# Optimization experiments

Hardware: AMD Instinct MI355X
Metric: run time of the kernel (lower is better)

Reference implementation:

```python
import jax, jax.numpy as jnp
import numpy as np
import math

NUM_HEADS = 32
NUM_KV_HEADS = 8
HEAD_DIM = 64
ROPE_THETA = 150000.0


def rotate_half(x):
    half = x.shape[-1] // 2
    return jnp.concatenate([-x[..., half:], x[..., :half]], axis=-1)


def setup_inputs() -> dict:
    key = jax.random.key(0)
    k1, k2, k3, k4, k5 = jax.random.split(key, 5)
    B, S, H = 2, 2048, 2048
    qkv_size = (NUM_HEADS + 2 * NUM_KV_HEADS) * HEAD_DIM  # 3072
    scale = 1.0 / math.sqrt(H)
    return {
        "hidden_states": jax.random.normal(k1, (B, S, H), jnp.float32),
        "position_ids": jnp.arange(S, dtype=jnp.int64 if jax.config.jax_enable_x64 else jnp.int32)[None, :],
        "qkv_w": jax.random.normal(k2, (qkv_size, H), jnp.float32) * scale,
        "qkv_b": jax.random.normal(k3, (qkv_size,), jnp.float32) * 0.01,
        "o_w": jax.random.normal(k4, (H, NUM_HEADS * HEAD_DIM), jnp.float32) * scale,
        "o_b": jax.random.normal(k5, (H,), jnp.float32) * 0.01,
    }


def reference(hidden_states, position_ids, qkv_w, qkv_b, o_w, o_b):
    B, S, _ = hidden_states.shape
    g = NUM_HEADS // NUM_KV_HEADS  # query heads per kv head
    d = HEAD_DIM

    qkv = hidden_states @ qkv_w.T + qkv_b  # [B,S,(H+2KV)*d]
    qkv = qkv.reshape(B, S, NUM_KV_HEADS, g + 2, d)
    q = qkv[:, :, :, :g, :].reshape(B, S, NUM_HEADS, d).transpose(0, 2, 1, 3)   # [B,Hq,S,d]
    k = qkv[:, :, :, g, :].transpose(0, 2, 1, 3)                                 # [B,Hkv,S,d]
    v = qkv[:, :, :, g + 1, :].transpose(0, 2, 1, 3)                             # [B,Hkv,S,d]

    # HF-style RoPE: cos/sin [S, d]
    inv_freq = 1.0 / (ROPE_THETA ** (jnp.arange(0, d, 2, dtype=jnp.float32) / d))
    freqs = jnp.outer(position_ids.reshape(-1).astype(jnp.float32), inv_freq)    # [S, d/2]
    emb = jnp.concatenate([freqs, freqs], axis=-1)                               # [S, d]
    cos = jnp.cos(emb)[None, None]                                               # [1,1,S,d]
    sin = jnp.sin(emb)[None, None]
    q = q * cos + rotate_half(q) * sin
    k = k * cos + rotate_half(k) * sin

    # GQA: repeat_interleave kv heads to match query heads
    k = jnp.repeat(k, g, axis=1)  # [B,Hq,S,d]
    v = jnp.repeat(v, g, axis=1)

    scores = jnp.einsum("bhqd,bhkd->bhqk", q, k) / math.sqrt(d)  # [B,Hq,S,S]
    attn = jax.nn.softmax(scores, axis=-1)
    out = jnp.einsum("bhqk,bhkd->bhqd", attn, v)
    out = out.transpose(0, 2, 1, 3).reshape(B, S, NUM_HEADS * d)
    return out @ o_w.T + o_b
```

## Files before the change

### kernel.cpp

```cpp
#include <hip/hip_runtime.h>
#include <math.h>

#define NHQ 32
#define NKV 8
#define HD 64
#define QKV_DIM 3072
#define MODEL_DIM 2048
#define QSCALE 0.1803368801111204f

typedef __attribute__((ext_vector_type(4))) float     f32x4;
typedef __attribute__((ext_vector_type(8))) _Float16  half8;
typedef __attribute__((ext_vector_type(4))) _Float16  half4v;
typedef __attribute__((ext_vector_type(2))) __fp16    fp16x2;
typedef __attribute__((ext_vector_type(4))) unsigned  uint32x4;

#define ASYNC_COPY16(g, l)                                                        \
    __builtin_amdgcn_global_load_lds(                                             \
        (const __attribute__((address_space(1))) void*)(g),                       \
        (__attribute__((address_space(3))) void*)(l), 16, 0, 0)

__device__ __forceinline__ float fast_exp2(float x)
{
#if __has_builtin(__builtin_amdgcn_exp2f)
    return __builtin_amdgcn_exp2f(x);
#else
    float r;
    asm volatile("v_exp_f32 %0, %1\ns_nop 0" : "=v"(r) : "v"(x));
    return r;
#endif
}

__global__ __launch_bounds__(256)
void f32_to_f16_kernel(const float* __restrict__ src, _Float16* __restrict__ dst, int n4)
{
    int i = blockIdx.x * 256 + threadIdx.x;
    if (i < n4) {
        float4 v = ((const float4*)src)[i];
        half4v h = { (_Float16)v.x, (_Float16)v.y, (_Float16)v.z, (_Float16)v.w };
        ((half4v*)dst)[i] = h;
    }
}

__global__ __launch_bounds__(256)
void sincos_table_kernel(const int* __restrict__ pos, float* __restrict__ tab, int S)
{
    int i = blockIdx.x * 256 + threadIdx.x;
    if (i < S * 32) {
        int s = i >> 5, fi = i & 31;
        float p = (float)pos[s];
        float inv_freq = powf(150000.0f, -(float)fi * (1.0f / 32.0f));
        float ang = p * inv_freq;
        tab[s * 64 + fi]      = cosf(ang);
        tab[s * 64 + 32 + fi] = sinf(ang);
    }
}

template<int MODE>
__global__ __launch_bounds__(256, 3)
void gemm_f16_mfma(const _Float16* __restrict__ A, const _Float16* __restrict__ W,
                   const float* __restrict__ bias, void* __restrict__ Cout,
                   const float* __restrict__ tab, int M, int N, int K, int S)
{
    __shared__ _Float16 As[3][128 * 32];
    __shared__ _Float16 Bs[3][128 * 32];

    const int t    = threadIdx.x;
    const int w    = t >> 6;
    const int lane = t & 63;
    const int quad = lane >> 4, l15 = lane & 15;
    const size_t m0 = (size_t)blockIdx.y * 128;
    const size_t n0 = (size_t)blockIdx.x * 128;
    const int wm = (w >> 1) * 64, wn = (w & 1) * 64;

    const int sr   = t >> 2;
    const int klog = ((t & 3) ^ ((sr >> 1) & 3)) * 8;
    const _Float16* ag0 = A + (m0 + sr) * K + klog;
    const _Float16* ag1 = A + (m0 + 64 + sr) * K + klog;
    const _Float16* bg0 = W + (n0 + sr) * K + klog;
    const _Float16* bg1 = W + (n0 + 64 + sr) * K + klog;

    const int xk8 = (quad ^ ((l15 >> 1) & 3)) * 8;

    f32x4 acc[4][4];
#pragma unroll
    for (int i = 0; i < 4; i++)
#pragma unroll
        for (int j = 0; j < 4; j++) acc[i][j] = (f32x4){0.f, 0.f, 0.f, 0.f};

    const int nt = K >> 5;

#define STAGE_TILE(bi, kt_)                                         \
    do {                                                            \
        const int _k0 = (kt_) * 32;                                 \
        ASYNC_COPY16(ag0 + _k0, &As[bi][w * 512]);                  \
        ASYNC_COPY16(ag1 + _k0, &As[bi][2048 + w * 512]);           \
        ASYNC_COPY16(bg0 + _k0, &Bs[bi][w * 512]);                  \
        ASYNC_COPY16(bg1 + _k0, &Bs[bi][2048 + w * 512]);           \
    } while (0)

    STAGE_TILE(0, 0);
    STAGE_TILE(1, 1);
    asm volatile("s_waitcnt vmcnt(4)" ::: "memory");
    __builtin_amdgcn_s_barrier();
    __builtin_amdgcn_sched_barrier(0);

    int bc = 0;
    for (int kt = 0; kt < nt; ++kt) {
        const _Float16* Ab = &As[bc][0];
        const _Float16* Bb = &Bs[bc][0];

        half8 af[4], bf[4];
#pragma unroll
        for (int i = 0; i < 4; i++) {
            af[i] = *(const half8*)(Ab + (wm + i * 16 + l15) * 32 + xk8);
            bf[i] = *(const half8*)(Bb + (wn + i * 16 + l15) * 32 + xk8);
        }

        if (kt + 2 < nt) {
            int bs = bc + 2; if (bs >= 3) bs -= 3;
            STAGE_TILE(bs, kt + 2);
        }

        __builtin_amdgcn_s_setprio(1);
#pragma unroll
        for (int i = 0; i < 4; i++)
#pragma unroll
            for (int j = 0; j < 4; j++)
                acc[i][j] = __builtin_amdgcn_mfma_f32_16x16x32_f16(af[i], bf[j], acc[i][j], 0, 0, 0);
        __builtin_amdgcn_s_setprio(0);

        if (kt + 1 < nt) {
            if (kt + 2 < nt) asm volatile("s_waitcnt vmcnt(4)" ::: "memory");
            else             asm volatile("s_waitcnt vmcnt(0)" ::: "memory");
            __builtin_amdgcn_s_barrier();
            __builtin_amdgcn_sched_barrier(0);
        }
        bc = bc + 1; if (bc == 3) bc = 0;
    }
#undef STAGE_TILE

    float bv[4];
#pragma unroll
    for (int j = 0; j < 4; j++) bv[j] = bias[n0 + wn + j * 16 + l15];

    const int ct = (int)(((n0 + wn) >> 6) % 6);

#pragma unroll
    for (int i = 0; i < 4; i++)
#pragma unroll
        for (int r = 0; r < 4; r++) {
            const size_t row = m0 + wm + i * 16 + quad * 4 + r;
            float v[4];
#pragma unroll
            for (int j = 0; j < 4; j++) v[j] = acc[i][j][r] + bv[j];

            if (MODE == 2 && ct != 5) {
                const float* tc = tab + (size_t)(row % S) * 64;
                const float ca = tc[l15],      sa = tc[32 + l15];
                const float cb = tc[16 + l15], sb = tc[48 + l15];
                const float qs = (ct < 4) ? QSCALE : 1.0f;
                const float n0v = v[0] * ca - v[2] * sa;
                const float n1v = v[1] * cb - v[3] * sb;
                const float n2v = v[2] * ca + v[0] * sa;
                const float n3v = v[3] * cb + v[1] * sb;
                v[0] = n0v * qs; v[1] = n1v * qs; v[2] = n2v * qs; v[3] = n3v * qs;
            }

            const size_t col = n0 + wn + l15;
#pragma unroll
            for (int j = 0; j < 4; j++) {
                if (MODE != 0) ((_Float16*)Cout)[row * N + col + j * 16] = (_Float16)v[j];
                else           ((float*)Cout)[row * N + col + j * 16] = v[j];
            }
        }
}

__global__ __launch_bounds__(256)
void transpose_v_kernel(const _Float16* __restrict__ qkv, _Float16* __restrict__ vtg, int BS)
{
    __shared__ _Float16 tile[64 * 72];
    const int t = threadIdx.x;
    const int tb = blockIdx.x * 64;
    const int g = blockIdx.y;
    const int voff = (g * 6 + 5) * 64;

    const int tok = t >> 2, dsub = (t & 3) * 16;
    const _Float16* src = qkv + (size_t)(tb + tok) * QKV_DIM + voff + dsub;
    *(half8*)&tile[tok * 72 + dsub]     = *(const half8*)(src);
    *(half8*)&tile[tok * 72 + dsub + 8] = *(const half8*)(src + 8);
    __syncthreads();

    const int d = t >> 2, tsub = (t & 3) * 16;
    half8 a, c;
#pragma unroll
    for (int i = 0; i < 8; i++) a[i] = tile[(tsub + i) * 72 + d];
#pragma unroll
    for (int i = 0; i < 8; i++) c[i] = tile[(tsub + 8 + i) * 72 + d];
    _Float16* dst = vtg + ((size_t)g * 64 + d) * BS + tb + tsub;
    *(half8*)dst       = a;
    *(half8*)(dst + 8) = c;
}

__global__ __launch_bounds__(256)
void attn_mfma(const _Float16* __restrict__ qkv, const _Float16* __restrict__ vtg,
               _Float16* __restrict__ out, int B, int S)
{
    __shared__ _Float16 Ks[64 * 72];
    __shared__ _Float16 VsT[64 * 72];

    const int t = threadIdx.x, w = t >> 6, lane = t & 63;
    const int quad = lane >> 4, l15 = lane & 15;
    const int b = blockIdx.z, g = blockIdx.y;
    const int q0 = blockIdx.x * 32;
    const int qoff = (g * 6 + w) * 64;
    const int koff = (g * 6 + 4) * 64;

    half8 qf[2][2];
#pragma unroll
    for (int s = 0; s < 2; s++) {
        const _Float16* qp = qkv + (size_t)(b * S + q0 + s * 16 + l15) * QKV_DIM + qoff;
        qf[s][0] = *(const half8*)(qp + quad * 8);
        qf[s][1] = *(const half8*)(qp + 32 + quad * 8);
    }

    half8 lv;
    {
        const _Float16 one = (l15 == 0) ? (_Float16)1.0f : (_Float16)0.0f;
#pragma unroll
        for (int j = 0; j < 8; j++) lv[j] = one;
    }

    f32x4 O[2][4], L[2];
#pragma unroll
    for (int s = 0; s < 2; s++) {
        L[s] = (f32x4){0.f, 0.f, 0.f, 0.f};
#pragma unroll
        for (int dt = 0; dt < 4; dt++) O[s][dt] = (f32x4){0.f, 0.f, 0.f, 0.f};
    }

    const int kst_tok = t >> 2;
    const int kst_d   = (t & 3) * 16;
    const int vst_d   = t >> 3;
    const int vst_sub = (t & 7) * 8;

    const _Float16* kbase  = qkv + (size_t)(b * S + kst_tok) * QKV_DIM + koff + kst_d;
    const _Float16* vbase0 = vtg + ((size_t)g * 64 + vst_d) * (size_t)(B * S) + b * S + vst_sub;
    const _Float16* vbase1 = vtg + ((size_t)g * 64 + 32 + vst_d) * (size_t)(B * S) + b * S + vst_sub;

    half8 kr0 = *(const half8*)(kbase);
    half8 kr1 = *(const half8*)(kbase + 8);
    half8 vr0 = *(const half8*)(vbase0);
    half8 vr1 = *(const half8*)(vbase1);

    for (int kt = 0; kt < S; kt += 64) {
        *(half8*)&Ks[kst_tok * 72 + kst_d]         = kr0;
        *(half8*)&Ks[kst_tok * 72 + kst_d + 8]     = kr1;
        *(half8*)&VsT[vst_d * 72 + vst_sub]        = vr0;
        *(half8*)&VsT[(32 + vst_d) * 72 + vst_sub] = vr1;
        __syncthreads();

        if (kt + 64 < S) {
            kr0 = *(const half8*)(kbase + (size_t)(kt + 64) * QKV_DIM);
            kr1 = *(const half8*)(kbase + (size_t)(kt + 64) * QKV_DIM + 8);
            vr0 = *(const half8*)(vbase0 + kt + 64);
            vr1 = *(const half8*)(vbase1 + kt + 64);
        }

        half8 kf[4][2];
#pragma unroll
        for (int mt = 0; mt < 4; mt++) {
            kf[mt][0] = *(const half8*)&Ks[(mt * 16 + l15) * 72 + quad * 8];
            kf[mt][1] = *(const half8*)&Ks[(mt * 16 + l15) * 72 + 32 + quad * 8];
        }

        half8 pf[2][2];
#pragma unroll
        for (int s = 0; s < 2; s++) {
            f32x4 sacc[4];
#pragma unroll
            for (int mt = 0; mt < 4; mt++) {
                f32x4 z = (f32x4){0.f, 0.f, 0.f, 0.f};
                z = __builtin_amdgcn_mfma_f32_16x16x32_f16(kf[mt][0], qf[s][0], z, 0, 0, 0);
                z = __builtin_amdgcn_mfma_f32_16x16x32_f16(kf[mt][1], qf[s][1], z, 0, 0, 0);
                sacc[mt] = z;
            }

            unsigned u[4][2];
#pragma unroll
            for (int mt = 0; mt < 4; mt++) {
                fp16x2 pa = __builtin_amdgcn_cvt_pkrtz(fast_exp2(sacc[mt][0]),
                                                       fast_exp2(sacc[mt][1]));
                fp16x2 pb = __builtin_amdgcn_cvt_pkrtz(fast_exp2(sacc[mt][2]),
                                                       fast_exp2(sacc[mt][3]));
                u[mt][0] = __builtin_bit_cast(unsigned, pa);
                u[mt][1] = __builtin_bit_cast(unsigned, pb);
            }

#pragma unroll
            for (int h = 0; h < 2; h++) {
                uint32x4 pw;
#pragma unroll
                for (int c = 0; c < 2; c++) {
                    unsigned x = u[h * 2][c], y = u[h * 2 + 1][c];
                    asm("v_permlane32_swap_b32 %0, %1" : "+v"(x), "+v"(y));
                    asm("v_permlane16_swap_b32 %0, %1" : "+v"(x), "+v"(y));
                    pw[c]     = x;
                    pw[2 + c] = y;
                }
                pf[s][h] = __builtin_bit_cast(half8, pw);
            }
        }

#pragma unroll
        for (int dt = 0; dt < 4; dt++) {
            half8 vv0 = *(const half8*)&VsT[(dt * 16 + l15) * 72 + quad * 8];
            half8 vv1 = *(const half8*)&VsT[(dt * 16 + l15) * 72 + 32 + quad * 8];
#pragma unroll
            for (int s = 0; s < 2; s++) {
                O[s][dt] = __builtin_amdgcn_mfma_f32_16x16x32_f16(pf[s][0], vv0, O[s][dt], 0, 0, 0);
                O[s][dt] = __builtin_amdgcn_mfma_f32_16x16x32_f16(pf[s][1], vv1, O[s][dt], 0, 0, 0);
            }
        }
#pragma unroll
        for (int s = 0; s < 2; s++) {
            L[s] = __builtin_amdgcn_mfma_f32_16x16x32_f16(pf[s][0], lv, L[s], 0, 0, 0);
            L[s] = __builtin_amdgcn_mfma_f32_16x16x32_f16(pf[s][1], lv, L[s], 0, 0, 0);
        }
        __syncthreads();
    }

    const int hq = g * 4 + w;
#pragma unroll
    for (int s = 0; s < 2; s++)
#pragma unroll
        for (int r = 0; r < 4; r++) {
            const float lr = __shfl(L[s][r], lane & 48, 64);
            const float ir = 1.0f / lr;
            const size_t row = (size_t)(b * S + q0 + s * 16 + quad * 4 + r);
#pragma unroll
            for (int dt = 0; dt < 4; dt++)
                out[row * (NHQ * HD) + hq * 64 + dt * 16 + l15] = (_Float16)(O[s][dt][r] * ir);
        }
}

extern "C" void kernel_launch(void* const* d_in, const int* in_sizes, int n_in,
                              void* d_out, int out_size, void* d_ws, size_t ws_size,
                              hipStream_t stream)
{
    const float* hidden = (const float*)d_in[0];
    const int*   pos    = (const int*)d_in[1];
    const float* qkv_w  = (const float*)d_in[2];
    const float* qkv_b  = (const float*)d_in[3];
    const float* o_w    = (const float*)d_in[4];
    const float* o_b    = (const float*)d_in[5];
    float* out = (float*)d_out;

    const int S  = in_sizes[1];
    const int BS = in_sizes[0] / MODEL_DIM;
    const int B  = BS / S;

    _Float16* hA   = (_Float16*)d_ws;
    _Float16* hW1  = hA   + (size_t)BS * MODEL_DIM;
    _Float16* hW2  = hW1  + (size_t)QKV_DIM * MODEL_DIM;
    _Float16* qkvh = hW2  + (size_t)MODEL_DIM * MODEL_DIM;
    _Float16* atth = qkvh + (size_t)BS * QKV_DIM;
    float*    tab  = (float*)(atth + (size_t)BS * MODEL_DIM);
    _Float16* vtg  = (_Float16*)(tab + (size_t)S * 64);

    f32_to_f16_kernel<<<(BS * MODEL_DIM / 4 + 255) / 256, 256, 0, stream>>>(hidden, hA, BS * MODEL_DIM / 4);
    f32_to_f16_kernel<<<(QKV_DIM * MODEL_DIM / 4 + 255) / 256, 256, 0, stream>>>(qkv_w, hW1, QKV_DIM * MODEL_DIM / 4);
    f32_to_f16_kernel<<<(MODEL_DIM * MODEL_DIM / 4 + 255) / 256, 256, 0, stream>>>(o_w, hW2, MODEL_DIM * MODEL_DIM / 4);
    sincos_table_kernel<<<(S * 32 + 255) / 256, 256, 0, stream>>>(pos, tab, S);

    gemm_f16_mfma<2><<<dim3(QKV_DIM / 128, BS / 128), 256, 0, stream>>>(
        hA, hW1, qkv_b, qkvh, tab, BS, QKV_DIM, MODEL_DIM, S);

    transpose_v_kernel<<<dim3(BS / 64, NKV), 256, 0, stream>>>(qkvh, vtg, BS);

    attn_mfma<<<dim3(S / 32, NKV, B), 256, 0, stream>>>(qkvh, vtg, atth, B, S);

    gemm_f16_mfma<0><<<dim3(MODEL_DIM / 128, BS / 128), 256, 0, stream>>>(
        atth, hW2, o_b, out, nullptr, BS, MODEL_DIM, MODEL_DIM, S);
}
```

Before: 314.9 us.

## Double-buffer attention K/V tiles, add MFMA priority hints, swizzle GEMM tile order

The attention kernel now keeps two LDS buffers for K and V^T. The next tile is written into the spare buffer while the current one is used for compute, which removes one __syncthreads per iteration and prefetches two tiles ahead. s_setprio is raised around the MFMA sections so the waves doing matrix work get scheduled first. The GEMM remaps block IDs using an XCD-aware interleave followed by grouped-M tile ordering, aiming for better L2 reuse across chiplets. Doubling LDS raises the attention kernel's shared-memory footprint, which could reduce occupancy.

```diff
diff --git a/kernel.cpp b/kernel.cpp
--- a/kernel.cpp
+++ b/kernel.cpp
@@ -68,8 +68,21 @@
     const int w    = t >> 6;
     const int lane = t & 63;
     const int quad = lane >> 4, l15 = lane & 15;
-    const size_t m0 = (size_t)blockIdx.y * 128;
-    const size_t n0 = (size_t)blockIdx.x * 128;
+
+    const int nnt = gridDim.x, nmt = gridDim.y;
+    int id = blockIdx.y * nnt + blockIdx.x;
+    const int nwg = nnt * nmt;
+    id = (id & 7) * (nwg >> 3) + (id >> 3);
+    const int GM  = 8;
+    const int npg = GM * nnt;
+    const int grp = id / npg;
+    const int fm  = grp * GM;
+    const int gsz = (nmt - fm < GM) ? (nmt - fm) : GM;
+    const int mtl = fm + (id % gsz);
+    const int ntl = (id % npg) / gsz;
+    const size_t m0 = (size_t)mtl * 128;
+    const size_t n0 = (size_t)ntl * 128;
+
     const int wm = (w >> 1) * 64, wn = (w & 1) * 64;
 
     const int sr   = t >> 2;
@@ -87,7 +100,7 @@
 #pragma unroll
         for (int j = 0; j < 4; j++) acc[i][j] = (f32x4){0.f, 0.f, 0.f, 0.f};
 
-    const int nt = K >> 5;
+    const int nkt = K >> 5;
 
 #define STAGE_TILE(bi, kt_)                                         \
     do {                                                            \
@@ -105,7 +118,7 @@
     __builtin_amdgcn_sched_barrier(0);
 
     int bc = 0;
-    for (int kt = 0; kt < nt; ++kt) {
+    for (int kt = 0; kt < nkt; ++kt) {
         const _Float16* Ab = &As[bc][0];
         const _Float16* Bb = &Bs[bc][0];
 
@@ -116,7 +129,7 @@
             bf[i] = *(const half8*)(Bb + (wn + i * 16 + l15) * 32 + xk8);
         }
 
-        if (kt + 2 < nt) {
+        if (kt + 2 < nkt) {
             int bs = bc + 2; if (bs >= 3) bs -= 3;
             STAGE_TILE(bs, kt + 2);
         }
@@ -129,8 +142,8 @@
                 acc[i][j] = __builtin_amdgcn_mfma_f32_16x16x32_f16(af[i], bf[j], acc[i][j], 0, 0, 0);
         __builtin_amdgcn_s_setprio(0);
 
-        if (kt + 1 < nt) {
-            if (kt + 2 < nt) asm volatile("s_waitcnt vmcnt(4)" ::: "memory");
+        if (kt + 1 < nkt) {
+            if (kt + 2 < nkt) asm volatile("s_waitcnt vmcnt(4)" ::: "memory");
             else             asm volatile("s_waitcnt vmcnt(0)" ::: "memory");
             __builtin_amdgcn_s_barrier();
             __builtin_amdgcn_sched_barrier(0);
@@ -205,8 +218,8 @@
 void attn_mfma(const _Float16* __restrict__ qkv, const _Float16* __restrict__ vtg,
                _Float16* __restrict__ out, int B, int S)
 {
-    __shared__ _Float16 Ks[64 * 72];
-    __shared__ _Float16 VsT[64 * 72];
+    __shared__ _Float16 Ks[2][64 * 72];
+    __shared__ _Float16 VsT[2][64 * 72];
 
     const int t = threadIdx.x, w = t >> 6, lane = t & 63;
     const int quad = lane >> 4, l15 = lane & 15;
@@ -251,32 +264,46 @@
     half8 kr1 = *(const half8*)(kbase + 8);
     half8 vr0 = *(const half8*)(vbase0);
     half8 vr1 = *(const half8*)(vbase1);
+    *(half8*)&Ks[0][kst_tok * 72 + kst_d]         = kr0;
+    *(half8*)&Ks[0][kst_tok * 72 + kst_d + 8]     = kr1;
+    *(half8*)&VsT[0][vst_d * 72 + vst_sub]        = vr0;
+    *(half8*)&VsT[0][(32 + vst_d) * 72 + vst_sub] = vr1;
+    __syncthreads();
+    if (64 < S) {
+        kr0 = *(const half8*)(kbase + (size_t)64 * QKV_DIM);
+        kr1 = *(const half8*)(kbase + (size_t)64 * QKV_DIM + 8);
+        vr0 = *(const half8*)(vbase0 + 64);
+        vr1 = *(const half8*)(vbase1 + 64);
+    }
 
     for (int kt = 0; kt < S; kt += 64) {
-        *(half8*)&Ks[kst_tok * 72 + kst_d]         = kr0;
-        *(half8*)&Ks[kst_tok * 72 + kst_d + 8]     = kr1;
-        *(half8*)&VsT[vst_d * 72 + vst_sub]        = vr0;
-        *(half8*)&VsT[(32 + vst_d) * 72 + vst_sub] = vr1;
-        __syncthreads();
+        const int c = (kt >> 6) & 1;
 
         if (kt + 64 < S) {
-            kr0 = *(const half8*)(kbase + (size_t)(kt + 64) * QKV_DIM);
-            kr1 = *(const half8*)(kbase + (size_t)(kt + 64) * QKV_DIM + 8);
-            vr0 = *(const half8*)(vbase0 + kt + 64);
-            vr1 = *(const half8*)(vbase1 + kt + 64);
+            *(half8*)&Ks[c ^ 1][kst_tok * 72 + kst_d]         = kr0;
+            *(half8*)&Ks[c ^ 1][kst_tok * 72 + kst_d + 8]     = kr1;
+            *(half8*)&VsT[c ^ 1][vst_d * 72 + vst_sub]        = vr0;
+            *(half8*)&VsT[c ^ 1][(32 + vst_d) * 72 + vst_sub] = vr1;
+        }
+        if (kt + 128 < S) {
+            kr0 = *(const half8*)(kbase + (size_t)(kt + 128) * QKV_DIM);
+            kr1 = *(const half8*)(kbase + (size_t)(kt + 128) * QKV_DIM + 8);
+            vr0 = *(const half8*)(vbase0 + kt + 128);
+            vr1 = *(const half8*)(vbase1 + kt + 128);
         }
 
         half8 kf[4][2];
 #pragma unroll
         for (int mt = 0; mt < 4; mt++) {
-            kf[mt][0] = *(const half8*)&Ks[(mt * 16 + l15) * 72 + quad * 8];
-            kf[mt][1] = *(const half8*)&Ks[(mt * 16 + l15) * 72 + 32 + quad * 8];
+            kf[mt][0] = *(const half8*)&Ks[c][(mt * 16 + l15) * 72 + quad * 8];
+            kf[mt][1] = *(const half8*)&Ks[c][(mt * 16 + l15) * 72 + 32 + quad * 8];
         }
 
         half8 pf[2][2];
 #pragma unroll
         for (int s = 0; s < 2; s++) {
             f32x4 sacc[4];
+            __builtin_amdgcn_s_setprio(1);
 #pragma unroll
             for (int mt = 0; mt < 4; mt++) {
                 f32x4 z = (f32x4){0.f, 0.f, 0.f, 0.f};
@@ -284,6 +311,7 @@
                 z = __builtin_amdgcn_mfma_f32_16x16x32_f16(kf[mt][1], qf[s][1], z, 0, 0, 0);
                 sacc[mt] = z;
             }
+            __builtin_amdgcn_s_setprio(0);
 
             unsigned u[4][2];
 #pragma unroll
@@ -300,21 +328,22 @@
             for (int h = 0; h < 2; h++) {
                 uint32x4 pw;
 #pragma unroll
-                for (int c = 0; c < 2; c++) {
-                    unsigned x = u[h * 2][c], y = u[h * 2 + 1][c];
+                for (int cc = 0; cc < 2; cc++) {
+                    unsigned x = u[h * 2][cc], y = u[h * 2 + 1][cc];
                     asm("v_permlane32_swap_b32 %0, %1" : "+v"(x), "+v"(y));
                     asm("v_permlane16_swap_b32 %0, %1" : "+v"(x), "+v"(y));
-                    pw[c]     = x;
-                    pw[2 + c] = y;
+                    pw[cc]     = x;
+                    pw[2 + cc] = y;
                 }
                 pf[s][h] = __builtin_bit_cast(half8, pw);
             }
         }
 
+        __builtin_amdgcn_s_setprio(1);
 #pragma unroll
         for (int dt = 0; dt < 4; dt++) {
-            half8 vv0 = *(const half8*)&VsT[(dt * 16 + l15) * 72 + quad * 8];
-            half8 vv1 = *(const half8*)&VsT[(dt * 16 + l15) * 72 + 32 + quad * 8];
+            half8 vv0 = *(const half8*)&VsT[c][(dt * 16 + l15) * 72 + quad * 8];
+            half8 vv1 = *(const half8*)&VsT[c][(dt * 16 + l15) * 72 + 32 + quad * 8];
 #pragma unroll
             for (int s = 0; s < 2; s++) {
                 O[s][dt] = __builtin_amdgcn_mfma_f32_16x16x32_f16(pf[s][0], vv0, O[s][dt], 0, 0, 0);
@@ -326,6 +355,8 @@
             L[s] = __builtin_amdgcn_mfma_f32_16x16x32_f16(pf[s][0], lv, L[s], 0, 0, 0);
             L[s] = __builtin_amdgcn_mfma_f32_16x16x32_f16(pf[s][1], lv, L[s], 0, 0, 0);
         }
+        __builtin_amdgcn_s_setprio(0);
+
         __syncthreads();
     }
 
```

Measured after the change: 323.6 us. 1.03x slower.

## Deepen GEMM LDS pipeline to four stages with register double-buffered fragments

Applied to the files above, without the earlier changes.

The GEMM moves from a 3-stage to a 4-stage LDS ring, prefetching three tiles ahead, and double-buffers the MFMA fragments in registers so the next tile's LDS reads overlap the current MFMAs. The loop is unrolled by two to alternate fragment buffers. The three fp32-to-fp16 conversion launches are merged into one kernel to save launch overhead. In exchange the kernel uses more LDS and registers, and the occupancy hint of 3 blocks per CU is dropped.

```diff
diff --git a/kernel.cpp b/kernel.cpp
--- a/kernel.cpp
+++ b/kernel.cpp
@@ -31,14 +31,26 @@
 }
 
 __global__ __launch_bounds__(256)
-void f32_to_f16_kernel(const float* __restrict__ src, _Float16* __restrict__ dst, int n4)
-{
-    int i = blockIdx.x * 256 + threadIdx.x;
-    if (i < n4) {
-        float4 v = ((const float4*)src)[i];
-        half4v h = { (_Float16)v.x, (_Float16)v.y, (_Float16)v.z, (_Float16)v.w };
-        ((half4v*)dst)[i] = h;
-    }
+void convert3_kernel(const float* __restrict__ s0, _Float16* __restrict__ d0, int n0,
+                     const float* __restrict__ s1, _Float16* __restrict__ d1, int n1,
+                     const float* __restrict__ s2, _Float16* __restrict__ d2, int n2)
+{
+    int j = blockIdx.x * 256 + threadIdx.x;
+    const float* s;
+    _Float16* d;
+    if (j < n0) { s = s0; d = d0; }
+    else {
+        j -= n0;
+        if (j < n1) { s = s1; d = d1; }
+        else {
+            j -= n1;
+            if (j >= n2) return;
+            s = s2; d = d2;
+        }
+    }
+    float4 v = ((const float4*)s)[j];
+    half4v h = { (_Float16)v.x, (_Float16)v.y, (_Float16)v.z, (_Float16)v.w };
+    ((half4v*)d)[j] = h;
 }
 
 __global__ __launch_bounds__(256)
@@ -56,13 +68,13 @@
 }
 
 template<int MODE>
-__global__ __launch_bounds__(256, 3)
+__global__ __launch_bounds__(256)
 void gemm_f16_mfma(const _Float16* __restrict__ A, const _Float16* __restrict__ W,
                    const float* __restrict__ bias, void* __restrict__ Cout,
                    const float* __restrict__ tab, int M, int N, int K, int S)
 {
-    __shared__ _Float16 As[3][128 * 32];
-    __shared__ _Float16 Bs[3][128 * 32];
+    __shared__ _Float16 As[4][128 * 32];
+    __shared__ _Float16 Bs[4][128 * 32];
 
     const int t    = threadIdx.x;
     const int w    = t >> 6;
@@ -87,7 +99,7 @@
 #pragma unroll
         for (int j = 0; j < 4; j++) acc[i][j] = (f32x4){0.f, 0.f, 0.f, 0.f};
 
-    const int nt = K >> 5;
+    const int nkt = K >> 5;
 
 #define STAGE_TILE(bi, kt_)                                         \
     do {                                                            \
@@ -98,45 +110,51 @@
         ASYNC_COPY16(bg1 + _k0, &Bs[bi][2048 + w * 512]);           \
     } while (0)
 
+#define LOAD_FRAGS(F, bi)                                                     \
+    do {                                                                      \
+        const _Float16* _Ab = &As[bi][0];                                     \
+        const _Float16* _Bb = &Bs[bi][0];                                     \
+        _Pragma("unroll")                                                     \
+        for (int i = 0; i < 4; i++) {                                         \
+            F[i]     = *(const half8*)(_Ab + (wm + i * 16 + l15) * 32 + xk8); \
+            F[4 + i] = *(const half8*)(_Bb + (wn + i * 16 + l15) * 32 + xk8); \
+        }                                                                     \
+    } while (0)
+
+#define KBODY(FC, FN, k)                                                      \
+    do {                                                                      \
+        if ((k) + 3 < nkt) STAGE_TILE(((k) + 3) & 3, (k) + 3);                \
+        if ((k) + 1 < nkt) LOAD_FRAGS(FN, ((k) + 1) & 3);                     \
+        __builtin_amdgcn_s_setprio(1);                                        \
+        _Pragma("unroll")                                                     \
+        for (int i = 0; i < 4; i++)                                           \
+            _Pragma("unroll")                                                 \
+            for (int j = 0; j < 4; j++)                                       \
+                acc[i][j] = __builtin_amdgcn_mfma_f32_16x16x32_f16(           \
+                    FC[i], FC[4 + j], acc[i][j], 0, 0, 0);                    \
+        __builtin_amdgcn_s_setprio(0);                                        \
+        if ((k) + 1 < nkt) {                                                  \
+            if ((k) + 3 < nkt) asm volatile("s_waitcnt vmcnt(4)" ::: "memory"); \
+            else               asm volatile("s_waitcnt vmcnt(0)" ::: "memory"); \
+            __builtin_amdgcn_s_barrier();                                     \
+            __builtin_amdgcn_sched_barrier(0);                                \
+        }                                                                     \
+    } while (0)
+
     STAGE_TILE(0, 0);
     STAGE_TILE(1, 1);
-    asm volatile("s_waitcnt vmcnt(4)" ::: "memory");
-    __builtin_amdgcn_s_barrier();
-    __builtin_amdgcn_sched_barrier(0);
-
-    int bc = 0;
-    for (int kt = 0; kt < nt; ++kt) {
-        const _Float16* Ab = &As[bc][0];
-        const _Float16* Bb = &Bs[bc][0];
-
-        half8 af[4], bf[4];
-#pragma unroll
-        for (int i = 0; i < 4; i++) {
-            af[i] = *(const half8*)(Ab + (wm + i * 16 + l15) * 32 + xk8);
-            bf[i] = *(const half8*)(Bb + (wn + i * 16 + l15) * 32 + xk8);
-        }
-
-        if (kt + 2 < nt) {
-            int bs = bc + 2; if (bs >= 3) bs -= 3;
-            STAGE_TILE(bs, kt + 2);
-        }
-
-        __builtin_amdgcn_s_setprio(1);
-#pragma unroll
-        for (int i = 0; i < 4; i++)
-#pragma unroll
-            for (int j = 0; j < 4; j++)
-                acc[i][j] = __builtin_amdgcn_mfma_f32_16x16x32_f16(af[i], bf[j], acc[i][j], 0, 0, 0);
-        __builtin_amdgcn_s_setprio(0);
-
-        if (kt + 1 < nt) {
-            if (kt + 2 < nt) asm volatile("s_waitcnt vmcnt(4)" ::: "memory");
-            else             asm volatile("s_waitcnt vmcnt(0)" ::: "memory");
-            __builtin_amdgcn_s_barrier();
-            __builtin_amdgcn_sched_barrier(0);
-        }
-        bc = bc + 1; if (bc == 3) bc = 0;
-    }
+    STAGE_TILE(2, 2);
+    __syncthreads();
+
+    half8 fA[8], fB[8];
+    LOAD_FRAGS(fA, 0);
+
+    for (int k = 0; k < nkt; k += 2) {
+        KBODY(fA, fB, k);
+        KBODY(fB, fA, k + 1);
+    }
+#undef KBODY
+#undef LOAD_FRAGS
 #undef STAGE_TILE
 
     float bv[4];
@@ -367,9 +385,11 @@
     float*    tab  = (float*)(atth + (size_t)BS * MODEL_DIM);
     _Float16* vtg  = (_Float16*)(tab + (size_t)S * 64);
 
-    f32_to_f16_kernel<<<(BS * MODEL_DIM / 4 + 255) / 256, 256, 0, stream>>>(hidden, hA, BS * MODEL_DIM / 4);
-    f32_to_f16_kernel<<<(QKV_DIM * MODEL_DIM / 4 + 255) / 256, 256, 0, stream>>>(qkv_w, hW1, QKV_DIM * MODEL_DIM / 4);
-    f32_to_f16_kernel<<<(MODEL_DIM * MODEL_DIM / 4 + 255) / 256, 256, 0, stream>>>(o_w, hW2, MODEL_DIM * MODEL_DIM / 4);
+    const int n0 = BS * MODEL_DIM / 4;
+    const int n1 = QKV_DIM * MODEL_DIM / 4;
+    const int n2 = MODEL_DIM * MODEL_DIM / 4;
+    convert3_kernel<<<(n0 + n1 + n2 + 255) / 256, 256, 0, stream>>>(
+        hidden, hA, n0, qkv_w, hW1, n1, o_w, hW2, n2);
     sincos_table_kernel<<<(S * 32 + 255) / 256, 256, 0, stream>>>(pos, tab, S);
 
     gemm_f16_mfma<2><<<dim3(QKV_DIM / 128, BS / 128), 256, 0, stream>>>(
```

Result: slower. 342.2 us (+8.7%).

## Double-buffer attention K/V tiles and merge prep kernels into one launch

Applied to the files above, without the earlier changes.

Attention now keeps two LDS buffers for K and V tiles. The next tile is written to shared memory while the current one is computed, so each iteration needs one barrier instead of two and global prefetch runs two tiles ahead. Separately, the three fp32-to-fp16 conversions and the sincos table are merged into a single prep kernel to save launch overhead. LDS use per block doubles, which could lower occupancy for the attention kernel.

```diff
diff --git a/kernel.cpp b/kernel.cpp
--- a/kernel.cpp
+++ b/kernel.cpp
@@ -31,27 +31,30 @@
 }
 
 __global__ __launch_bounds__(256)
-void f32_to_f16_kernel(const float* __restrict__ src, _Float16* __restrict__ dst, int n4)
-{
-    int i = blockIdx.x * 256 + threadIdx.x;
-    if (i < n4) {
-        float4 v = ((const float4*)src)[i];
+void prep_kernel(const float* __restrict__ s0, _Float16* __restrict__ d0, int n0,
+                 const float* __restrict__ s1, _Float16* __restrict__ d1, int n1,
+                 const float* __restrict__ s2, _Float16* __restrict__ d2, int n2,
+                 const int* __restrict__ pos, float* __restrict__ tab, int ns)
+{
+    int j = blockIdx.x * 256 + threadIdx.x;
+    if (j < n0 + n1 + n2) {
+        const float* s; _Float16* d;
+        if (j < n0)           { s = s0; d = d0; }
+        else if (j < n0 + n1) { s = s1; d = d1; j -= n0; }
+        else                  { s = s2; d = d2; j -= n0 + n1; }
+        float4 v = ((const float4*)s)[j];
         half4v h = { (_Float16)v.x, (_Float16)v.y, (_Float16)v.z, (_Float16)v.w };
-        ((half4v*)dst)[i] = h;
-    }
-}
-
-__global__ __launch_bounds__(256)
-void sincos_table_kernel(const int* __restrict__ pos, float* __restrict__ tab, int S)
-{
-    int i = blockIdx.x * 256 + threadIdx.x;
-    if (i < S * 32) {
-        int s = i >> 5, fi = i & 31;
-        float p = (float)pos[s];
-        float inv_freq = powf(150000.0f, -(float)fi * (1.0f / 32.0f));
-        float ang = p * inv_freq;
-        tab[s * 64 + fi]      = cosf(ang);
-        tab[s * 64 + 32 + fi] = sinf(ang);
+        ((half4v*)d)[j] = h;
+    } else {
+        j -= n0 + n1 + n2;
+        if (j < ns) {
+            int s = j >> 5, fi = j & 31;
+            float p = (float)pos[s];
+            float inv_freq = powf(150000.0f, -(float)fi * (1.0f / 32.0f));
+            float ang = p * inv_freq;
+            tab[s * 64 + fi]      = cosf(ang);
+            tab[s * 64 + 32 + fi] = sinf(ang);
+        }
     }
 }
 
@@ -87,7 +90,7 @@
 #pragma unroll
         for (int j = 0; j < 4; j++) acc[i][j] = (f32x4){0.f, 0.f, 0.f, 0.f};
 
-    const int nt = K >> 5;
+    const int nkt = K >> 5;
 
 #define STAGE_TILE(bi, kt_)                                         \
     do {                                                            \
@@ -105,7 +108,7 @@
     __builtin_amdgcn_sched_barrier(0);
 
     int bc = 0;
-    for (int kt = 0; kt < nt; ++kt) {
+    for (int kt = 0; kt < nkt; ++kt) {
         const _Float16* Ab = &As[bc][0];
         const _Float16* Bb = &Bs[bc][0];
 
@@ -116,7 +119,7 @@
             bf[i] = *(const half8*)(Bb + (wn + i * 16 + l15) * 32 + xk8);
         }
 
-        if (kt + 2 < nt) {
+        if (kt + 2 < nkt) {
             int bs = bc + 2; if (bs >= 3) bs -= 3;
             STAGE_TILE(bs, kt + 2);
         }
@@ -129,9 +132,9 @@
                 acc[i][j] = __builtin_amdgcn_mfma_f32_16x16x32_f16(af[i], bf[j], acc[i][j], 0, 0, 0);
         __builtin_amdgcn_s_setprio(0);
 
-        if (kt + 1 < nt) {
-            if (kt + 2 < nt) asm volatile("s_waitcnt vmcnt(4)" ::: "memory");
-            else             asm volatile("s_waitcnt vmcnt(0)" ::: "memory");
+        if (kt + 1 < nkt) {
+            if (kt + 2 < nkt) asm volatile("s_waitcnt vmcnt(4)" ::: "memory");
+            else              asm volatile("s_waitcnt vmcnt(0)" ::: "memory");
             __builtin_amdgcn_s_barrier();
             __builtin_amdgcn_sched_barrier(0);
         }
@@ -205,8 +208,8 @@
 void attn_mfma(const _Float16* __restrict__ qkv, const _Float16* __restrict__ vtg,
                _Float16* __restrict__ out, int B, int S)
 {
-    __shared__ _Float16 Ks[64 * 72];
-    __shared__ _Float16 VsT[64 * 72];
+    __shared__ _Float16 Ks[2][64 * 72];
+    __shared__ _Float16 VsT[2][64 * 72];
 
     const int t = threadIdx.x, w = t >> 6, lane = t & 63;
     const int quad = lane >> 4, l15 = lane & 15;
@@ -247,87 +250,103 @@
     const _Float16* vbase0 = vtg + ((size_t)g * 64 + vst_d) * (size_t)(B * S) + b * S + vst_sub;
     const _Float16* vbase1 = vtg + ((size_t)g * 64 + 32 + vst_d) * (size_t)(B * S) + b * S + vst_sub;
 
+    const int NT = S >> 6;
+
     half8 kr0 = *(const half8*)(kbase);
     half8 kr1 = *(const half8*)(kbase + 8);
     half8 vr0 = *(const half8*)(vbase0);
     half8 vr1 = *(const half8*)(vbase1);
-
-    for (int kt = 0; kt < S; kt += 64) {
-        *(half8*)&Ks[kst_tok * 72 + kst_d]         = kr0;
-        *(half8*)&Ks[kst_tok * 72 + kst_d + 8]     = kr1;
-        *(half8*)&VsT[vst_d * 72 + vst_sub]        = vr0;
-        *(half8*)&VsT[(32 + vst_d) * 72 + vst_sub] = vr1;
-        __syncthreads();
-
-        if (kt + 64 < S) {
-            kr0 = *(const half8*)(kbase + (size_t)(kt + 64) * QKV_DIM);
-            kr1 = *(const half8*)(kbase + (size_t)(kt + 64) * QKV_DIM + 8);
-            vr0 = *(const half8*)(vbase0 + kt + 64);
-            vr1 = *(const half8*)(vbase1 + kt + 64);
-        }
-
-        half8 kf[4][2];
-#pragma unroll
-        for (int mt = 0; mt < 4; mt++) {
-            kf[mt][0] = *(const half8*)&Ks[(mt * 16 + l15) * 72 + quad * 8];
-            kf[mt][1] = *(const half8*)&Ks[(mt * 16 + l15) * 72 + 32 + quad * 8];
-        }
-
-        half8 pf[2][2];
-#pragma unroll
-        for (int s = 0; s < 2; s++) {
-            f32x4 sacc[4];
-#pragma unroll
-            for (int mt = 0; mt < 4; mt++) {
-                f32x4 z = (f32x4){0.f, 0.f, 0.f, 0.f};
-                z = __builtin_amdgcn_mfma_f32_16x16x32_f16(kf[mt][0], qf[s][0], z, 0, 0, 0);
-                z = __builtin_amdgcn_mfma_f32_16x16x32_f16(kf[mt][1], qf[s][1], z, 0, 0, 0);
-                sacc[mt] = z;
-            }
-
-            unsigned u[4][2];
-#pragma unroll
-            for (int mt = 0; mt < 4; mt++) {
-                fp16x2 pa = __builtin_amdgcn_cvt_pkrtz(fast_exp2(sacc[mt][0]),
-                                                       fast_exp2(sacc[mt][1]));
-                fp16x2 pb = __builtin_amdgcn_cvt_pkrtz(fast_exp2(sacc[mt][2]),
-                                                       fast_exp2(sacc[mt][3]));
-                u[mt][0] = __builtin_bit_cast(unsigned, pa);
-                u[mt][1] = __builtin_bit_cast(unsigned, pb);
-            }
-
-#pragma unroll
-            for (int h = 0; h < 2; h++) {
-                uint32x4 pw;
-#pragma unroll
-                for (int c = 0; c < 2; c++) {
-                    unsigned x = u[h * 2][c], y = u[h * 2 + 1][c];
-                    asm("v_permlane32_swap_b32 %0, %1" : "+v"(x), "+v"(y));
-                    asm("v_permlane16_swap_b32 %0, %1" : "+v"(x), "+v"(y));
-                    pw[c]     = x;
-                    pw[2 + c] = y;
-                }
-                pf[s][h] = __builtin_bit_cast(half8, pw);
-            }
-        }
-
-#pragma unroll
-        for (int dt = 0; dt < 4; dt++) {
-            half8 vv0 = *(const half8*)&VsT[(dt * 16 + l15) * 72 + quad * 8];
-            half8 vv1 = *(const half8*)&VsT[(dt * 16 + l15) * 72 + 32 + quad * 8];
-#pragma unroll
-            for (int s = 0; s < 2; s++) {
-                O[s][dt] = __builtin_amdgcn_mfma_f32_16x16x32_f16(pf[s][0], vv0, O[s][dt], 0, 0, 0);
-                O[s][dt] = __builtin_amdgcn_mfma_f32_16x16x32_f16(pf[s][1], vv1, O[s][dt], 0, 0, 0);
-            }
-        }
-#pragma unroll
-        for (int s = 0; s < 2; s++) {
-            L[s] = __builtin_amdgcn_mfma_f32_16x16x32_f16(pf[s][0], lv, L[s], 0, 0, 0);
-            L[s] = __builtin_amdgcn_mfma_f32_16x16x32_f16(pf[s][1], lv, L[s], 0, 0, 0);
-        }
-        __syncthreads();
-    }
+    *(half8*)&Ks[0][kst_tok * 72 + kst_d]         = kr0;
+    *(half8*)&Ks[0][kst_tok * 72 + kst_d + 8]     = kr1;
+    *(half8*)&VsT[0][vst_d * 72 + vst_sub]        = vr0;
+    *(half8*)&VsT[0][(32 + vst_d) * 72 + vst_sub] = vr1;
+    kr0 = *(const half8*)(kbase + (size_t)64 * QKV_DIM);
+    kr1 = *(const half8*)(kbase + (size_t)64 * QKV_DIM + 8);
+    vr0 = *(const half8*)(vbase0 + 64);
+    vr1 = *(const half8*)(vbase1 + 64);
+    asm volatile("s_waitcnt lgkmcnt(0)" ::: "memory");
+    __builtin_amdgcn_s_barrier();
+
+#define ATTN_TILE(CUR, NXT, TT)                                                    \
+    do {                                                                           \
+        half8 kf[4][2];                                                            \
+        _Pragma("unroll")                                                          \
+        for (int mt = 0; mt < 4; mt++) {                                           \
+            kf[mt][0] = *(const half8*)&Ks[CUR][(mt * 16 + l15) * 72 + quad * 8];  \
+            kf[mt][1] = *(const half8*)&Ks[CUR][(mt * 16 + l15) * 72 + 32 + quad * 8]; \
+        }                                                                          \
+        if ((TT) + 1 < NT) {                                                       \
+            *(half8*)&Ks[NXT][kst_tok * 72 + kst_d]         = kr0;                 \
+            *(half8*)&Ks[NXT][kst_tok * 72 + kst_d + 8]     = kr1;                 \
+            *(half8*)&VsT[NXT][vst_d * 72 + vst_sub]        = vr0;                 \
+            *(half8*)&VsT[NXT][(32 + vst_d) * 72 + vst_sub] = vr1;                 \
+        }                                                                          \
+        if ((TT) + 2 < NT) {                                                       \
+            const size_t off = (size_t)((TT) + 2) * 64;                            \
+            kr0 = *(const half8*)(kbase + off * QKV_DIM);                          \
+            kr1 = *(const half8*)(kbase + off * QKV_DIM + 8);                      \
+            vr0 = *(const half8*)(vbase0 + off);                                   \
+            vr1 = *(const half8*)(vbase1 + off);                                   \
+        }                                                                          \
+        half8 pf[2][2];                                                            \
+        _Pragma("unroll")                                                          \
+        for (int s = 0; s < 2; s++) {                                              \
+            f32x4 sacc[4];                                                         \
+            _Pragma("unroll")                                                      \
+            for (int mt = 0; mt < 4; mt++) {                                       \
+                f32x4 z = (f32x4){0.f, 0.f, 0.f, 0.f};                             \
+                z = __builtin_amdgcn_mfma_f32_16x16x32_f16(kf[mt][0], qf[s][0], z, 0, 0, 0); \
+                z = __builtin_amdgcn_mfma_f32_16x16x32_f16(kf[mt][1], qf[s][1], z, 0, 0, 0); \
+                sacc[mt] = z;                                                      \
+            }                                                                      \
+            unsigned u[4][2];                                                      \
+            _Pragma("unroll")                                                      \
+            for (int mt = 0; mt < 4; mt++) {                                       \
+                fp16x2 pa = __builtin_amdgcn_cvt_pkrtz(fast_exp2(sacc[mt][0]),     \
+                                                       fast_exp2(sacc[mt][1]));    \
+                fp16x2 pb = __builtin_amdgcn_cvt_pkrtz(fast_exp2(sacc[mt][2]),     \
+                                                       fast_exp2(sacc[mt][3]));    \
+                u[mt][0] = __builtin_bit_cast(unsigned, pa);                       \
+                u[mt][1] = __builtin_bit_cast(unsigned, pb);                       \
+            }                                                                      \
+            _Pragma("unroll")                                                      \
+            for (int h = 0; h < 2; h++) {                                          \
+                uint32x4 pw;                                                       \
+                _Pragma("unroll")                                                  \
+                for (int cc = 0; cc < 2; cc++) {                                   \
+                    unsigned x = u[h * 2][cc], y = u[h * 2 + 1][cc];               \
+                    asm("v_permlane32_swap_b32 %0, %1" : "+v"(x), "+v"(y));        \
+                    asm("v_permlane16_swap_b32 %0, %1" : "+v"(x), "+v"(y));        \
+                    pw[cc]     = x;                                                \
+                    pw[2 + cc] = y;                                                \
+                }                                                                  \
+                pf[s][h] = __builtin_bit_cast(half8, pw);                          \
+            }                                                                      \
+        }                                                                          \
+        _Pragma("unroll")                                                          \
+        for (int dt = 0; dt < 4; dt++) {                                           \
+            half8 vv0 = *(const half8*)&VsT[CUR][(dt * 16 + l15) * 72 + quad * 8]; \
+            half8 vv1 = *(const half8*)&VsT[CUR][(dt * 16 + l15) * 72 + 32 + quad * 8]; \
+            _Pragma("unroll")                                                      \
+            for (int s = 0; s < 2; s++) {                                          \
+                O[s][dt] = __builtin_amdgcn_mfma_f32_16x16x32_f16(pf[s][0], vv0, O[s][dt], 0, 0, 0); \
+                O[s][dt] = __builtin_amdgcn_mfma_f32_16x16x32_f16(pf[s][1], vv1, O[s][dt], 0, 0, 0); \
+            }                                                                      \
+        }                                                                          \
+        _Pragma("unroll")                                                          \
+        for (int s = 0; s < 2; s++) {                                              \
+            L[s] = __builtin_amdgcn_mfma_f32_16x16x32_f16(pf[s][0], lv, L[s], 0, 0, 0); \
+            L[s] = __builtin_amdgcn_mfma_f32_16x16x32_f16(pf[s][1], lv, L[s], 0, 0, 0); \
+        }                                                                          \
+        asm volatile("s_waitcnt lgkmcnt(0)" ::: "memory");                         \
+        __builtin_amdgcn_s_barrier();                                              \
+    } while (0)
+
+    for (int tt = 0; tt < NT; tt += 2) {
+        ATTN_TILE(0, 1, tt);
+        ATTN_TILE(1, 0, tt + 1);
+    }
+#undef ATTN_TILE
 
     const int hq = g * 4 + w;
 #pragma unroll
@@ -367,10 +386,12 @@
     float*    tab  = (float*)(atth + (size_t)BS * MODEL_DIM);
     _Float16* vtg  = (_Float16*)(tab + (size_t)S * 64);
 
-    f32_to_f16_kernel<<<(BS * MODEL_DIM / 4 + 255) / 256, 256, 0, stream>>>(hidden, hA, BS * MODEL_DIM / 4);
-    f32_to_f16_kernel<<<(QKV_DIM * MODEL_DIM / 4 + 255) / 256, 256, 0, stream>>>(qkv_w, hW1, QKV_DIM * MODEL_DIM / 4);
-    f32_to_f16_kernel<<<(MODEL_DIM * MODEL_DIM / 4 + 255) / 256, 256, 0, stream>>>(o_w, hW2, MODEL_DIM * MODEL_DIM / 4);
-    sincos_table_kernel<<<(S * 32 + 255) / 256, 256, 0, stream>>>(pos, tab, S);
+    const int n0 = BS * MODEL_DIM / 4;
+    const int n1 = QKV_DIM * MODEL_DIM / 4;
+    const int n2 = MODEL_DIM * MODEL_DIM / 4;
+    const int ns = S * 32;
+    prep_kernel<<<(n0 + n1 + n2 + ns + 255) / 256, 256, 0, stream>>>(
+        hidden, hA, n0, qkv_w, hW1, n1, o_w, hW2, n2, pos, tab, ns);
 
     gemm_f16_mfma<2><<<dim3(QKV_DIM / 128, BS / 128), 256, 0, stream>>>(
         hA, hW1, qkv_b, qkvh, tab, BS, QKV_DIM, MODEL_DIM, S);
```

Measured after the change: 322.9 us. 2.5% more time.
